# Optimization experiments

Hardware: AMD Instinct MI355X
Metric: run time of the kernel (lower is better)

Reference implementation:

```python
import jax, jax.numpy as jnp
import numpy as np

B, N, C, H = 4, 1024, 768, 12
D = C // H  # head dim = 64
SCALE = D ** -0.5


def setup_inputs() -> dict:
    key = jax.random.key(0)
    ks = jax.random.split(key, 13)
    inp = {
        'q': jax.random.normal(ks[0], (N, B, C), jnp.float32),
        'k': jax.random.normal(ks[1], (N, B, C), jnp.float32),
        'v': jax.random.normal(ks[2], (N, B, C), jnp.float32),
        'attn_mask': jax.random.randint(ks[3], (B, N), 0, 2).astype(bool),
        'Wq': jax.random.normal(ks[4], (C, C), jnp.float32) * 0.02,
        'bq': jax.random.normal(ks[5], (C,), jnp.float32) * 0.02,
        'Wk': jax.random.normal(ks[6], (C, C), jnp.float32) * 0.02,
        'bk': jax.random.normal(ks[7], (C,), jnp.float32) * 0.02,
        'Wv': jax.random.normal(ks[8], (C, C), jnp.float32) * 0.02,
        'bv': jax.random.normal(ks[9], (C,), jnp.float32) * 0.02,
        'Wo': jax.random.normal(ks[10], (C, C), jnp.float32) * 0.02,
        'bo': jax.random.normal(ks[11], (C,), jnp.float32) * 0.02,
        'zeta': jnp.ones((1, H, 1, D), jnp.float32),  # orig (1,1,H,1,D); leading 1 dropped by [0]
    }
    return inp


def reference(q, k, v, attn_mask, Wq, bq, Wk, bk, Wv, bv, Wo, bo, zeta):
    # inputs are [N, B, C]; module permutes to [B, N, C]
    q = q.transpose(1, 0, 2)
    k = k.transpose(1, 0, 2)
    v = v.transpose(1, 0, 2)
    b, n_q, c = q.shape
    n_k = k.shape[1]

    def heads(x, W, bias):
        y = x @ W.T + bias                          # [B, N, C]
        return y.reshape(b, -1, H, D).transpose(0, 2, 1, 3)  # [B, H, N, D]

    qh = heads(q, Wq, bq) * zeta
    kh = heads(k, Wk, bk) * zeta
    vh = heads(v, Wv, bv) * zeta

    scores = jnp.einsum('bhqd,bhkd->bhqk', qh, kh)
    mask_add = jnp.where(attn_mask[:, None, None, :], -jnp.inf, 0.0).astype(scores.dtype)
    # torch path: baddbmm(mask, q, k^T) * scale -> (qk + mask) * scale
    attn = jax.nn.softmax((scores + mask_add) * SCALE, axis=-1)

    x = jnp.einsum('bhqk,bhkd->bhqd', attn, vh)
    x = x.transpose(0, 2, 1, 3).reshape(b, n_q, c)  # [B, N_q, C]
    x = x @ Wo.T + bo
    return x.transpose(1, 0, 2)  # back to [N_q, B, C]
```

## Files before the change

### kernel.cpp

```cpp
#include <hip/hip_runtime.h>
#include <cstdint>
#include <cstddef>

typedef unsigned short us;
using short8 = __attribute__((ext_vector_type(8))) short;
using f32x4  = __attribute__((ext_vector_type(4))) float;

union U8 { us u[8]; short8 v; };
union PU { int w[4]; short8 v; };

#define MFMA16(a,b,c) __builtin_amdgcn_mfma_f32_16x16x32_bf16((a),(b),(c),0,0,0)

static __device__ __forceinline__ us f2bf(float f){
  union { float f; unsigned u; } cv; cv.f = f;
  unsigned u = cv.u;
  return (us)((u + 0x7fffu + ((u >> 16) & 1u)) >> 16);
}

static __device__ __forceinline__ int base_of(const int* nbd, int b){
  int s = 0;
#pragma unroll
  for (int i = 0; i < 3; ++i) if (i < b) s += (nbd[i] + 127) & ~127;
  return s;
}

typedef const __attribute__((address_space(1))) void* gp_t;
typedef __attribute__((address_space(3))) void* lp_t;
#define GL16(g,l) __builtin_amdgcn_global_load_lds((gp_t)(g),(lp_t)(l),16,0,0)

__global__ __launch_bounds__(256) void prep_a(
    const float* __restrict__ Wq, const float* __restrict__ Wk,
    const float* __restrict__ Wv, const float* __restrict__ Wo,
    const int* __restrict__ mask,
    us* __restrict__ wb, f32x4* __restrict__ zreg,
    int* __restrict__ rank, int* __restrict__ nbd)
{
  const int bid = blockIdx.x, tid = threadIdx.x;
  if (bid < 4){
    const int b = bid, lane = tid & 63, w = tid >> 6;
    __shared__ int wsum[4];
    int m[4], cnt = 0;
#pragma unroll
    for (int j = 0; j < 4; ++j){
      m[j] = mask[b * 1024 + tid * 4 + j] ? 0 : 1;
      cnt += m[j];
    }
    int sc = cnt;
#pragma unroll
    for (int off = 1; off < 64; off <<= 1){
      int t = __shfl_up(sc, off, 64);
      if (lane >= off) sc += t;
    }
    if (lane == 63) wsum[w] = sc;
    __syncthreads();
    int woff = 0;
#pragma unroll
    for (int i = 0; i < 4; ++i) if (i < w) woff += wsum[i];
    const int total = wsum[0] + wsum[1] + wsum[2] + wsum[3];
    int rr = woff + sc - cnt;
#pragma unroll
    for (int j = 0; j < 4; ++j){
      rank[b * 1024 + tid * 4 + j] = m[j] ? rr : -1;
      rr += m[j];
    }
    if (tid == 0) nbd[b] = total;
  } else if (bid < 1156){
    unsigned wi = (bid - 4) * 256u + tid;
    unsigned z  = wi / 73728u;
    unsigned rr = wi - z * 73728u;
    const float* W = (z == 0) ? Wq : (z == 1) ? Wk : (z == 2) ? Wv : Wo;
    const float* src = W + (size_t)rr * 8u;
    f32x4 a = *(const f32x4*)src;
    f32x4 b = *(const f32x4*)(src + 4);
    U8 o;
#pragma unroll
    for (int j = 0; j < 4; ++j){ o.u[j] = f2bf(a[j]); o.u[4 + j] = f2bf(b[j]); }
    *(short8*)(wb + (size_t)z * 589824u + rr * 8u) = o.v;
  } else {
    zreg[(size_t)(bid - 1156) * 256 + tid] = f32x4{};
  }
}

__global__ __launch_bounds__(256) void prep_b(
    const float* __restrict__ xq, const float* __restrict__ xk, const float* __restrict__ xv,
    const int* __restrict__ rank, const int* __restrict__ nbd,
    us* __restrict__ xbq, us* __restrict__ xbk, us* __restrict__ xbv)
{
  unsigned id = blockIdx.x * 256u + threadIdx.x;
  unsigned z  = id / 393216u;
  unsigned rr = id - z * 393216u;
  unsigned row = rr / 96u, cc = rr - row * 96u;
  unsigned bsel = row >> 10, n = row & 1023u;
  const float* src; us* dst;
  if (z == 0){
    src = xq  + (size_t)(n * 4u + bsel) * 768u + cc * 8u;
    dst = xbq + (size_t)row * 768u + cc * 8u;
  } else {
    int rk = rank[row];
    if (rk < 0) return;
    int grow = base_of(nbd, (int)bsel) + rk;
    const float* x = (z == 1) ? xk : xv;
    us* xb = (z == 1) ? xbk : xbv;
    src = x  + (size_t)(n * 4u + bsel) * 768u + cc * 8u;
    dst = xb + (size_t)grow * 768u + cc * 8u;
  }
  f32x4 a = *(const f32x4*)src;
  f32x4 b = *(const f32x4*)(src + 4);
  U8 o;
#pragma unroll
  for (int j = 0; j < 4; ++j){ o.u[j] = f2bf(a[j]); o.u[4 + j] = f2bf(b[j]); }
  *(short8*)dst = o.v;
}

__global__ __launch_bounds__(256, 2) void qkv_gemm7(
    const us* __restrict__ xbq, const us* __restrict__ xbk, const us* __restrict__ xbv,
    const us* __restrict__ wb,
    const float* __restrict__ bq, const float* __restrict__ bk, const float* __restrict__ bv,
    const float* __restrict__ zeta, const int* __restrict__ nbd,
    us* __restrict__ qh, us* __restrict__ kc, us* __restrict__ vtc)
{
  const int z = blockIdx.z;
  int mt, nt;
  if (z == 0){
    const int flat = blockIdx.x + blockIdx.y * 32;
    const int xcd = flat & 7, c = flat >> 3;
    mt = xcd * 4 + (c & 3);
    nt = c >> 2;
  } else {
    const int mtv = (base_of(nbd, 3) + ((nbd[3] + 127) & ~127)) >> 7;
    const int nlive = 6 * mtv;
    const int c = blockIdx.x + blockIdx.y * 32;
    const int xcd = c & 7, j = c >> 3;
    const int qd = nlive >> 3, rm = nlive & 7;
    const int cnt = qd + (xcd < rm ? 1 : 0);
    if (j >= cnt) return;
    const int start = xcd * qd + (xcd < rm ? xcd : rm);
    const int wk = start + j;
    mt = wk / 6;
    nt = wk - mt * 6;
  }
  const us* A  = (z == 0) ? xbq : (z == 1) ? xbk : xbv;
  const us* Bw = wb + (size_t)z * 589824;
  const float* bias = (z == 0) ? bq : (z == 1) ? bk : bv;

  __shared__ __align__(16) us As[2][128 * 64];
  __shared__ __align__(16) us Bs[2][128 * 64];

  const int tid = threadIdx.x, lane = tid & 63, w = tid >> 6;
  const int wr = (w >> 1) * 64, wc = (w & 1) * 64;

  f32x4 acc[4][4] = {};

  auto STAGE = [&](int kt, int buf){
#pragma unroll
    for (int p = 0; p < 4; ++p){
      int chunk = p * 256 + tid;
      int row = chunk >> 3;
      int colb = ((chunk & 7) ^ (row & 7)) * 8;
      GL16(A  + (size_t)(mt * 128 + row) * 768 + kt * 64 + colb,
           As[buf] + (p * 256 + w * 64) * 8);
      GL16(Bw + (size_t)(nt * 128 + row) * 768 + kt * 64 + colb,
           Bs[buf] + (p * 256 + w * 64) * 8);
    }
  };

  STAGE(0, 0);
  STAGE(1, 1);
  for (int kt = 0; kt < 12; ++kt){
    const int cur = kt & 1;
    if (kt < 11) asm volatile("s_waitcnt vmcnt(8)" ::: "memory");
    else         asm volatile("s_waitcnt vmcnt(0)" ::: "memory");
    __builtin_amdgcn_s_barrier();

#pragma unroll
    for (int ks = 0; ks < 2; ++ks){
      short8 af[4], bf4[4];
#pragma unroll
      for (int mf = 0; mf < 4; ++mf){
        int row = wr + mf * 16 + (lane & 15);
        int byte = (row * 128 + ks * 64 + (lane >> 4) * 16) ^ ((row & 7) << 4);
        af[mf] = *(const short8*)((const char*)As[cur] + byte);
      }
#pragma unroll
      for (int nf = 0; nf < 4; ++nf){
        int row = wc + nf * 16 + (lane & 15);
        int byte = (row * 128 + ks * 64 + (lane >> 4) * 16) ^ ((row & 7) << 4);
        bf4[nf] = *(const short8*)((const char*)Bs[cur] + byte);
      }
#pragma unroll
      for (int mf = 0; mf < 4; ++mf)
#pragma unroll
        for (int nf = 0; nf < 4; ++nf)
          acc[mf][nf] = MFMA16(af[mf], bf4[nf], acc[mf][nf]);
    }

    asm volatile("s_waitcnt lgkmcnt(0)" ::: "memory");
    __builtin_amdgcn_s_barrier();
    if (kt < 10) STAGE(kt + 2, cur);
  }

  float bzv[4], zzv[4]; int colv[4];
#pragma unroll
  for (int nf = 0; nf < 4; ++nf){
    colv[nf] = nt * 128 + wc + nf * 16 + (lane & 15);
    bzv[nf] = bias[colv[nf]];
    zzv[nf] = zeta[colv[nf]];
  }

  if (z == 0){
#pragma unroll
    for (int mf = 0; mf < 4; ++mf)
#pragma unroll
      for (int r = 0; r < 4; ++r){
        int row = mt * 128 + wr + mf * 16 + (lane >> 4) * 4 + r;
#pragma unroll
        for (int nf = 0; nf < 4; ++nf)
          qh[(size_t)row * 768 + colv[nf]] = f2bf((acc[mf][nf][r] + bzv[nf]) * zzv[nf]);
      }
  } else {
    const int row0 = mt * 128;
    const int b0 = base_of(nbd, 1), b1 = base_of(nbd, 2), b2 = base_of(nbd, 3);
    const int bsel = (row0 >= b0) + (row0 >= b1) + (row0 >= b2);
    const int base_b = (bsel == 0) ? 0 : (bsel == 1) ? b0 : (bsel == 2) ? b1 : b2;
    const int nb = nbd[bsel];
#pragma unroll
    for (int mf = 0; mf < 4; ++mf)
#pragma unroll
      for (int r = 0; r < 4; ++r){
        int grow = mt * 128 + wr + mf * 16 + (lane >> 4) * 4 + r;
        int row_local = grow - base_b;
        if (row_local >= nb) continue;
        if (z == 1){
#pragma unroll
          for (int nf = 0; nf < 4; ++nf)
            kc[(size_t)grow * 768 + colv[nf]] =
                f2bf((acc[mf][nf][r] + bzv[nf]) * zzv[nf]);
        } else {
#pragma unroll
          for (int nf = 0; nf < 4; ++nf){
            int hh = colv[nf] >> 6, dd = colv[nf] & 63;
            vtc[((size_t)(bsel * 12 + hh) * 64 + dd) * 1024 + row_local] =
                f2bf((acc[mf][nf][r] + bzv[nf]) * zzv[nf]);
          }
        }
      }
  }
}

__global__ __launch_bounds__(256) void attn_fwd6(
    const us* __restrict__ qh, const us* __restrict__ kc,
    const us* __restrict__ vtc, const int* __restrict__ nbd,
    us* __restrict__ ao)
{
  const int flat = blockIdx.x + 16 * blockIdx.y + 192 * blockIdx.z;
  const int xcd = flat & 7, c = flat >> 3;
  const int pair = xcd * 6 + (c >> 4);
  const int qt = c & 15, h = pair % 12, b = pair / 12;
  const int tid = threadIdx.x, lane = tid & 63, w = tid >> 6;

  const int nbv = nbd[b];
  const int base_b = base_of(nbd, b);
  const int nt = (nbv + 63) >> 6;

  __shared__ __align__(16) us Ks[2][64 * 64];
  __shared__ __align__(16) us Vs[2][64 * 64];

  short8 qf[2];
#pragma unroll
  for (int ks = 0; ks < 2; ++ks)
    qf[ks] = *(const short8*)(qh +
              (size_t)(b * 1024 + qt * 64 + w * 16 + (lane & 15)) * 768 +
              h * 64 + ks * 32 + (lane >> 4) * 8);

  short8 kr[2], vr[2];
  auto KVLOAD = [&](int kt){
#pragma unroll
    for (int p = 0; p < 2; ++p){
      int cc = p * 256 + tid, row = cc >> 3, db = (cc & 7) * 8;
      kr[p] = *(const short8*)(kc + (size_t)(base_b + kt * 64 + row) * 768 + h * 64 + db);
      vr[p] = *(const short8*)(vtc + ((size_t)((b * 12 + h) * 64 + row)) * 1024 + kt * 64 + db);
    }
  };
  auto KVWRITE = [&](int buf){
#pragma unroll
    for (int p = 0; p < 2; ++p){
      int cc = p * 256 + tid, row = cc >> 3, db = (cc & 7) * 8;
      int byte = (row * 128 + db * 2) ^ ((row & 7) << 4);
      *(short8*)((char*)Ks[buf] + byte) = kr[p];
      *(short8*)((char*)Vs[buf] + byte) = vr[p];
    }
  };
  KVLOAD(0); KVWRITE(0);
  __syncthreads();

  const int bpbase = (((lane & 16) << 1) | (lane & 15)) << 2;
  const bool hi5 = (lane & 32) != 0;

  float lsum = 0.f;
  f32x4 o[4] = {};
  int cur = 0;
  for (int kt = 0; kt < nt; ++kt){
    if (kt + 1 < nt) KVLOAD(kt + 1);

    f32x4 s[4] = {};
#pragma unroll
    for (int ks = 0; ks < 2; ++ks)
#pragma unroll
      for (int f = 0; f < 4; ++f){
        int row = f * 16 + (lane & 15);
        short8 kf = *(const short8*)((const char*)Ks[cur] +
                    ((row * 128 + ks * 64 + (lane >> 4) * 16) ^ ((row & 7) << 4)));
        s[f] = MFMA16(kf, qf[ks], s[f]);
      }

    float p_[4][4];
#pragma unroll
    for (int f = 0; f < 4; ++f)
#pragma unroll
      for (int r = 0; r < 4; ++r)
        p_[f][r] = __expf(s[f][r] * 0.125f);
    if (kt == nt - 1){
      int kb = kt * 64 + ((lane >> 4) << 2);
#pragma unroll
      for (int f = 0; f < 4; ++f)
#pragma unroll
        for (int r = 0; r < 4; ++r)
          p_[f][r] = (kb + f * 16 + r < nbv) ? p_[f][r] : 0.f;
    }
#pragma unroll
    for (int f = 0; f < 4; ++f)
      lsum += (p_[f][0] + p_[f][1]) + (p_[f][2] + p_[f][3]);

    unsigned pk[4][2];
#pragma unroll
    for (int f = 0; f < 4; ++f){
      pk[f][0] = (unsigned)f2bf(p_[f][0]) | ((unsigned)f2bf(p_[f][1]) << 16);
      pk[f][1] = (unsigned)f2bf(p_[f][2]) | ((unsigned)f2bf(p_[f][3]) << 16);
    }

    PU pa0, pa1;
#pragma unroll
    for (int j = 0; j < 4; ++j){
      int addr = bpbase + ((j & 2) << 5);
      int wsel = j & 1;
      int t0 = __builtin_amdgcn_ds_bpermute(addr, (int)pk[0][wsel]);
      int t1 = __builtin_amdgcn_ds_bpermute(addr, (int)pk[1][wsel]);
      int t2 = __builtin_amdgcn_ds_bpermute(addr, (int)pk[2][wsel]);
      int t3 = __builtin_amdgcn_ds_bpermute(addr, (int)pk[3][wsel]);
      pa0.w[j] = hi5 ? t1 : t0;
      pa1.w[j] = hi5 ? t3 : t2;
    }

#pragma unroll
    for (int df = 0; df < 4; ++df){
      int vrow = df * 16 + (lane & 15);
      short8 vb0 = *(const short8*)((const char*)Vs[cur] +
                   ((vrow * 128 + 0  + (lane >> 4) * 16) ^ ((vrow & 7) << 4)));
      short8 vb1 = *(const short8*)((const char*)Vs[cur] +
                   ((vrow * 128 + 64 + (lane >> 4) * 16) ^ ((vrow & 7) << 4)));
      o[df] = MFMA16(pa0.v, vb0, o[df]);
      o[df] = MFMA16(pa1.v, vb1, o[df]);
    }

    if (kt + 1 < nt) KVWRITE(cur ^ 1);
    __syncthreads();
    cur ^= 1;
  }

  float l = lsum;
  l += __shfl_xor(l, 16, 64);
  l += __shfl_xor(l, 32, 64);
  float linv[4];
#pragma unroll
  for (int r = 0; r < 4; ++r)
    linv[r] = __builtin_amdgcn_rcpf(__shfl(l, (lane >> 4) * 4 + r, 64));

#pragma unroll
  for (int df = 0; df < 4; ++df)
#pragma unroll
    for (int r = 0; r < 4; ++r){
      int qrow = qt * 64 + w * 16 + (lane >> 4) * 4 + r;
      int dcol = df * 16 + (lane & 15);
      ao[(size_t)(b * 1024 + qrow) * 768 + h * 64 + dcol] = f2bf(o[df][r] * linv[r]);
    }
}

__global__ __launch_bounds__(256, 2) void out_gemm4(
    const us* __restrict__ ain, const us* __restrict__ wo,
    const float* __restrict__ bo, float* __restrict__ dout)
{
  __shared__ __align__(16) us As[2][128 * 64];
  __shared__ __align__(16) us Bs[2][128 * 64];

  const int tid = threadIdx.x, lane = tid & 63, w = tid >> 6;
  const int wr = (w >> 1) * 64, wc = (w & 1) * 64;
  const int flat = blockIdx.x + blockIdx.y * 32;
  const int xcd = flat & 7, c = flat >> 3;
  const int mt = xcd * 4 + (c & 3);
  const int nt = c >> 2;

  f32x4 acc[4][4] = {};

  auto STAGE = [&](int kt, int buf){
#pragma unroll
    for (int p = 0; p < 4; ++p){
      int chunk = p * 256 + tid;
      int row = chunk >> 3;
      int colb = ((chunk & 7) ^ (row & 7)) * 8;
      GL16(ain + (size_t)(mt * 128 + row) * 768 + kt * 64 + colb,
           As[buf] + (p * 256 + w * 64) * 8);
      GL16(wo  + (size_t)(nt * 128 + row) * 768 + kt * 64 + colb,
           Bs[buf] + (p * 256 + w * 64) * 8);
    }
  };

  STAGE(0, 0);
  STAGE(1, 1);
  for (int kt = 0; kt < 12; ++kt){
    const int cur = kt & 1;
    if (kt < 11) asm volatile("s_waitcnt vmcnt(8)" ::: "memory");
    else         asm volatile("s_waitcnt vmcnt(0)" ::: "memory");
    __builtin_amdgcn_s_barrier();

#pragma unroll
    for (int ks = 0; ks < 2; ++ks){
      short8 af[4], bf4[4];
#pragma unroll
      for (int mf = 0; mf < 4; ++mf){
        int row = wr + mf * 16 + (lane & 15);
        int byte = (row * 128 + ks * 64 + (lane >> 4) * 16) ^ ((row & 7) << 4);
        af[mf] = *(const short8*)((const char*)As[cur] + byte);
      }
#pragma unroll
      for (int nf = 0; nf < 4; ++nf){
        int row = wc + nf * 16 + (lane & 15);
        int byte = (row * 128 + ks * 64 + (lane >> 4) * 16) ^ ((row & 7) << 4);
        bf4[nf] = *(const short8*)((const char*)Bs[cur] + byte);
      }
#pragma unroll
      for (int mf = 0; mf < 4; ++mf)
#pragma unroll
        for (int nf = 0; nf < 4; ++nf)
          acc[mf][nf] = MFMA16(af[mf], bf4[nf], acc[mf][nf]);
    }

    asm volatile("s_waitcnt lgkmcnt(0)" ::: "memory");
    __builtin_amdgcn_s_barrier();
    if (kt < 10) STAGE(kt + 2, cur);
  }

#pragma unroll
  for (int nf = 0; nf < 4; ++nf){
    int col = nt * 128 + wc + nf * 16 + (lane & 15);
    float bz = bo[col];
#pragma unroll
    for (int mf = 0; mf < 4; ++mf)
#pragma unroll
      for (int r = 0; r < 4; ++r){
        int row = mt * 128 + wr + mf * 16 + (lane >> 4) * 4 + r;
        int n = row & 1023, bsel = row >> 10;
        dout[(size_t)(n * 4 + bsel) * 768 + col] = acc[mf][nf][r] + bz;
      }
  }
}

extern "C" void kernel_launch(void* const* d_in, const int* in_sizes, int n_in,
                              void* d_out, int out_size, void* d_ws, size_t ws_size,
                              hipStream_t stream)
{
  const float* q    = (const float*)d_in[0];
  const float* k    = (const float*)d_in[1];
  const float* v    = (const float*)d_in[2];
  const int*   mask = (const int*)d_in[3];
  const float* Wq   = (const float*)d_in[4];
  const float* bq   = (const float*)d_in[5];
  const float* Wk   = (const float*)d_in[6];
  const float* bk   = (const float*)d_in[7];
  const float* Wv   = (const float*)d_in[8];
  const float* bv   = (const float*)d_in[9];
  const float* Wo   = (const float*)d_in[10];
  const float* bo   = (const float*)d_in[11];
  const float* zeta = (const float*)d_in[12];

  us* xbq = (us*)d_out;
  us* xbk = xbq + 3145728;
  us* xbv = (us*)d_ws;
  us* wb  = xbv + 3145728;
  us* qh  = wb  + 2359296;
  us* kc  = qh  + 3145728;
  us* vtc = kc  + 3145728;
  int* rank = (int*)(vtc + 3145728);
  int* nbd  = rank + 4096;
  us* ao = xbv;

  prep_a<<<4228, 256, 0, stream>>>(Wq, Wk, Wv, Wo, mask, wb, (f32x4*)kc, rank, nbd);
  prep_b<<<4608, 256, 0, stream>>>(q, k, v, rank, nbd, xbq, xbk, xbv);
  qkv_gemm7<<<dim3(32, 6, 3), 256, 0, stream>>>(xbq, xbk, xbv, wb, bq, bk, bv,
                                                zeta, nbd, qh, kc, vtc);
  attn_fwd6<<<dim3(16, 12, 4), 256, 0, stream>>>(qh, kc, vtc, nbd, ao);
  out_gemm4<<<dim3(32, 6, 1), 256, 0, stream>>>(ao, wb + 3 * 589824, bo, (float*)d_out);
}
```

Baseline: 73.53 us.

## Use 512-thread QKV GEMM blocks, rebalance prep kernels, add MFMA priority hints

The QKV projection GEMM now runs 8 waves per 128x128 tile instead of 4, so each wave holds a 32x64 slab of the output. This halves per-wave accumulators and gives more waves to hide latency, at the cost of one block per CU and more LDS-fragment reloads of B. The q fp32->bf16 conversion moves from prep_b into prep_a, and only the V cache is zeroed now, which shifts work between the two prep launches. The attention kernel wraps its MFMA sections in s_setprio to favour matrix issue across waves.

```diff
diff --git a/kernel.cpp b/kernel.cpp
--- a/kernel.cpp
+++ b/kernel.cpp
@@ -29,10 +29,11 @@
 #define GL16(g,l) __builtin_amdgcn_global_load_lds((gp_t)(g),(lp_t)(l),16,0,0)
 
 __global__ __launch_bounds__(256) void prep_a(
+    const float* __restrict__ xq,
     const float* __restrict__ Wq, const float* __restrict__ Wk,
     const float* __restrict__ Wv, const float* __restrict__ Wo,
     const int* __restrict__ mask,
-    us* __restrict__ wb, f32x4* __restrict__ zreg,
+    us* __restrict__ xbq, us* __restrict__ wb, f32x4* __restrict__ zreg,
     int* __restrict__ rank, int* __restrict__ nbd)
 {
   const int bid = blockIdx.x, tid = threadIdx.x;
@@ -64,46 +65,49 @@
       rr += m[j];
     }
     if (tid == 0) nbd[b] = total;
-  } else if (bid < 1156){
+    return;
+  }
+  const float* src; us* dst;
+  if (bid < 1156){
     unsigned wi = (bid - 4) * 256u + tid;
     unsigned z  = wi / 73728u;
     unsigned rr = wi - z * 73728u;
     const float* W = (z == 0) ? Wq : (z == 1) ? Wk : (z == 2) ? Wv : Wo;
-    const float* src = W + (size_t)rr * 8u;
-    f32x4 a = *(const f32x4*)src;
-    f32x4 b = *(const f32x4*)(src + 4);
-    U8 o;
-#pragma unroll
-    for (int j = 0; j < 4; ++j){ o.u[j] = f2bf(a[j]); o.u[4 + j] = f2bf(b[j]); }
-    *(short8*)(wb + (size_t)z * 589824u + rr * 8u) = o.v;
+    src = W  + (size_t)rr * 8u;
+    dst = wb + (size_t)z * 589824u + rr * 8u;
+  } else if (bid < 2692){
+    unsigned id = (bid - 1156) * 256u + tid;
+    unsigned row = id / 96u, cc = id - row * 96u;
+    unsigned bsel = row >> 10, n = row & 1023u;
+    src = xq  + (size_t)(n * 4u + bsel) * 768u + cc * 8u;
+    dst = xbq + (size_t)row * 768u + cc * 8u;
   } else {
-    zreg[(size_t)(bid - 1156) * 256 + tid] = f32x4{};
-  }
+    zreg[(size_t)(bid - 2692) * 256 + tid] = f32x4{};
+    return;
+  }
+  f32x4 a = *(const f32x4*)src;
+  f32x4 b = *(const f32x4*)(src + 4);
+  U8 o;
+#pragma unroll
+  for (int j = 0; j < 4; ++j){ o.u[j] = f2bf(a[j]); o.u[4 + j] = f2bf(b[j]); }
+  *(short8*)dst = o.v;
 }
 
 __global__ __launch_bounds__(256) void prep_b(
-    const float* __restrict__ xq, const float* __restrict__ xk, const float* __restrict__ xv,
+    const float* __restrict__ xk, const float* __restrict__ xv,
     const int* __restrict__ rank, const int* __restrict__ nbd,
-    us* __restrict__ xbq, us* __restrict__ xbk, us* __restrict__ xbv)
+    us* __restrict__ xbk, us* __restrict__ xbv)
 {
   unsigned id = blockIdx.x * 256u + threadIdx.x;
   unsigned z  = id / 393216u;
   unsigned rr = id - z * 393216u;
   unsigned row = rr / 96u, cc = rr - row * 96u;
   unsigned bsel = row >> 10, n = row & 1023u;
-  const float* src; us* dst;
-  if (z == 0){
-    src = xq  + (size_t)(n * 4u + bsel) * 768u + cc * 8u;
-    dst = xbq + (size_t)row * 768u + cc * 8u;
-  } else {
-    int rk = rank[row];
-    if (rk < 0) return;
-    int grow = base_of(nbd, (int)bsel) + rk;
-    const float* x = (z == 1) ? xk : xv;
-    us* xb = (z == 1) ? xbk : xbv;
-    src = x  + (size_t)(n * 4u + bsel) * 768u + cc * 8u;
-    dst = xb + (size_t)grow * 768u + cc * 8u;
-  }
+  int rk = rank[row];
+  if (rk < 0) return;
+  int grow = base_of(nbd, (int)bsel) + rk;
+  const float* src = ((z == 0) ? xk : xv) + (size_t)(n * 4u + bsel) * 768u + cc * 8u;
+  us* dst = ((z == 0) ? xbk : xbv) + (size_t)grow * 768u + cc * 8u;
   f32x4 a = *(const f32x4*)src;
   f32x4 b = *(const f32x4*)(src + 4);
   U8 o;
@@ -112,7 +116,7 @@
   *(short8*)dst = o.v;
 }
 
-__global__ __launch_bounds__(256, 2) void qkv_gemm7(
+__global__ __launch_bounds__(512, 1) void qkv_gemm8(
     const us* __restrict__ xbq, const us* __restrict__ xbk, const us* __restrict__ xbv,
     const us* __restrict__ wb,
     const float* __restrict__ bq, const float* __restrict__ bk, const float* __restrict__ bv,
@@ -147,20 +151,20 @@
   __shared__ __align__(16) us Bs[2][128 * 64];
 
   const int tid = threadIdx.x, lane = tid & 63, w = tid >> 6;
-  const int wr = (w >> 1) * 64, wc = (w & 1) * 64;
-
-  f32x4 acc[4][4] = {};
+  const int wr = (w >> 1) * 32, wc = (w & 1) * 64;
+
+  f32x4 acc[2][4] = {};
 
   auto STAGE = [&](int kt, int buf){
 #pragma unroll
-    for (int p = 0; p < 4; ++p){
-      int chunk = p * 256 + tid;
+    for (int p = 0; p < 2; ++p){
+      int chunk = p * 512 + tid;
       int row = chunk >> 3;
       int colb = ((chunk & 7) ^ (row & 7)) * 8;
       GL16(A  + (size_t)(mt * 128 + row) * 768 + kt * 64 + colb,
-           As[buf] + (p * 256 + w * 64) * 8);
+           As[buf] + (p * 512 + w * 64) * 8);
       GL16(Bw + (size_t)(nt * 128 + row) * 768 + kt * 64 + colb,
-           Bs[buf] + (p * 256 + w * 64) * 8);
+           Bs[buf] + (p * 512 + w * 64) * 8);
     }
   };
 
@@ -168,15 +172,15 @@
   STAGE(1, 1);
   for (int kt = 0; kt < 12; ++kt){
     const int cur = kt & 1;
-    if (kt < 11) asm volatile("s_waitcnt vmcnt(8)" ::: "memory");
+    if (kt < 11) asm volatile("s_waitcnt vmcnt(4)" ::: "memory");
     else         asm volatile("s_waitcnt vmcnt(0)" ::: "memory");
     __builtin_amdgcn_s_barrier();
 
 #pragma unroll
     for (int ks = 0; ks < 2; ++ks){
-      short8 af[4], bf4[4];
-#pragma unroll
-      for (int mf = 0; mf < 4; ++mf){
+      short8 af[2], bf4[4];
+#pragma unroll
+      for (int mf = 0; mf < 2; ++mf){
         int row = wr + mf * 16 + (lane & 15);
         int byte = (row * 128 + ks * 64 + (lane >> 4) * 16) ^ ((row & 7) << 4);
         af[mf] = *(const short8*)((const char*)As[cur] + byte);
@@ -188,7 +192,7 @@
         bf4[nf] = *(const short8*)((const char*)Bs[cur] + byte);
       }
 #pragma unroll
-      for (int mf = 0; mf < 4; ++mf)
+      for (int mf = 0; mf < 2; ++mf)
 #pragma unroll
         for (int nf = 0; nf < 4; ++nf)
           acc[mf][nf] = MFMA16(af[mf], bf4[nf], acc[mf][nf]);
@@ -209,7 +213,7 @@
 
   if (z == 0){
 #pragma unroll
-    for (int mf = 0; mf < 4; ++mf)
+    for (int mf = 0; mf < 2; ++mf)
 #pragma unroll
       for (int r = 0; r < 4; ++r){
         int row = mt * 128 + wr + mf * 16 + (lane >> 4) * 4 + r;
@@ -224,7 +228,7 @@
     const int base_b = (bsel == 0) ? 0 : (bsel == 1) ? b0 : (bsel == 2) ? b1 : b2;
     const int nb = nbd[bsel];
 #pragma unroll
-    for (int mf = 0; mf < 4; ++mf)
+    for (int mf = 0; mf < 2; ++mf)
 #pragma unroll
       for (int r = 0; r < 4; ++r){
         int grow = mt * 128 + wr + mf * 16 + (lane >> 4) * 4 + r;
@@ -247,7 +251,7 @@
   }
 }
 
-__global__ __launch_bounds__(256) void attn_fwd6(
+__global__ __launch_bounds__(256) void attn_fwd7(
     const us* __restrict__ qh, const us* __restrict__ kc,
     const us* __restrict__ vtc, const int* __restrict__ nbd,
     us* __restrict__ ao)
@@ -303,6 +307,7 @@
     if (kt + 1 < nt) KVLOAD(kt + 1);
 
     f32x4 s[4] = {};
+    __builtin_amdgcn_s_setprio(1);
 #pragma unroll
     for (int ks = 0; ks < 2; ++ks)
 #pragma unroll
@@ -312,6 +317,7 @@
                     ((row * 128 + ks * 64 + (lane >> 4) * 16) ^ ((row & 7) << 4)));
         s[f] = MFMA16(kf, qf[ks], s[f]);
       }
+    __builtin_amdgcn_s_setprio(0);
 
     float p_[4][4];
 #pragma unroll
@@ -351,6 +357,7 @@
       pa1.w[j] = hi5 ? t3 : t2;
     }
 
+    __builtin_amdgcn_s_setprio(1);
 #pragma unroll
     for (int df = 0; df < 4; ++df){
       int vrow = df * 16 + (lane & 15);
@@ -361,6 +368,7 @@
       o[df] = MFMA16(pa0.v, vb0, o[df]);
       o[df] = MFMA16(pa1.v, vb1, o[df]);
     }
+    __builtin_amdgcn_s_setprio(0);
 
     if (kt + 1 < nt) KVWRITE(cur ^ 1);
     __syncthreads();
@@ -493,10 +501,11 @@
   int* nbd  = rank + 4096;
   us* ao = xbv;
 
-  prep_a<<<4228, 256, 0, stream>>>(Wq, Wk, Wv, Wo, mask, wb, (f32x4*)kc, rank, nbd);
-  prep_b<<<4608, 256, 0, stream>>>(q, k, v, rank, nbd, xbq, xbk, xbv);
-  qkv_gemm7<<<dim3(32, 6, 3), 256, 0, stream>>>(xbq, xbk, xbv, wb, bq, bk, bv,
+  prep_a<<<4228, 256, 0, stream>>>(q, Wq, Wk, Wv, Wo, mask,
+                                   xbq, wb, (f32x4*)vtc, rank, nbd);
+  prep_b<<<3072, 256, 0, stream>>>(k, v, rank, nbd, xbk, xbv);
+  qkv_gemm8<<<dim3(32, 6, 3), 512, 0, stream>>>(xbq, xbk, xbv, wb, bq, bk, bv,
                                                 zeta, nbd, qh, kc, vtc);
-  attn_fwd6<<<dim3(16, 12, 4), 256, 0, stream>>>(qh, kc, vtc, nbd, ao);
+  attn_fwd7<<<dim3(16, 12, 4), 256, 0, stream>>>(qh, kc, vtc, nbd, ao);
   out_gemm4<<<dim3(32, 6, 1), 256, 0, stream>>>(ao, wb + 3 * 589824, bo, (float*)d_out);
 }
```

Result: faster. 68.92 us (-6.3%).
